# Kernel optimization log

Hardware: AMD Instinct MI355X
Metric: run time of the kernel (lower is better)

The kernel has to match this reference:

```python
import jax, jax.numpy as jnp
import numpy as np

N = 8192
F_IN = 256
F_OUT = 64
ALPHA = 0.2  # leaky-relu negative slope
NEG_INF = -9e15


def setup_inputs() -> dict:
    key = jax.random.key(0)
    k1, k2, k3, k4 = jax.random.split(key, 4)
    h = jax.random.normal(k1, (N, F_IN), dtype=jnp.float32)
    adj = jax.random.randint(k2, (N, N), 0, 2, dtype=jnp.int32)
    W = jax.random.normal(k3, (F_IN, F_OUT), dtype=jnp.float32)
    a = jax.random.normal(k4, (2 * F_OUT, 1), dtype=jnp.float32)
    return {"h": h, "adj": adj, "W": W, "a": a}


def reference(h, adj, W, a):
    # Wh: [N, F_OUT]
    Wh = h @ W
    # Decompose a = [a1; a2]: e_ij = leakyrelu(a1^T Wh_i + a2^T Wh_j),
    # identical math to concat([Wh_i, Wh_j]) @ a without the O(N^2*2F) tensor.
    a1 = a[:F_OUT, 0]
    a2 = a[F_OUT:, 0]
    s1 = Wh @ a1  # [N]
    s2 = Wh @ a2  # [N]
    e = s1[:, None] + s2[None, :]  # [N, N]
    e = jnp.where(e > 0, e, ALPHA * e)  # leaky relu
    scores = jnp.where(adj > 0, e, NEG_INF)
    attention = jax.nn.softmax(scores, axis=1)  # [N, N]
    h_prime = attention @ Wh  # [N, F_OUT]
    return h_prime
```

## Files before the change

kernel.cpp:

```cpp
#include <hip/hip_runtime.h>

#define N 8192
#define F_IN 256
#define F_OUT 64
#define ALPHA 0.2f
#define LOG2E 1.4426950408889634f
#define NEGBIG -3.0e38f
#define MINIT -1.0e30f

typedef __attribute__((ext_vector_type(8))) short bf16x8;
typedef __attribute__((ext_vector_type(4))) float f32x4;
typedef __attribute__((ext_vector_type(4))) int i32x4;
typedef __attribute__((ext_vector_type(4))) unsigned u32x4;
typedef __attribute__((ext_vector_type(4))) unsigned short u16x4;

__device__ __forceinline__ unsigned short f2bf(float x) {
    unsigned u = __float_as_uint(x);
    u = (u + 0x7FFFu + ((u >> 16) & 1u)) >> 16;
    return (unsigned short)u;
}
__device__ __forceinline__ float bf2f(unsigned short h) {
    return __uint_as_float((unsigned)h << 16);
}
__device__ __forceinline__ float fast_exp2(float x) {
#if __has_builtin(__builtin_amdgcn_exp2f)
    return __builtin_amdgcn_exp2f(x);
#else
    return __expf(x * 0.6931471805599453f);
#endif
}
__device__ __forceinline__ i32x4 ntload4(const int* p) {
    return __builtin_nontemporal_load((const i32x4*)p);
}

__global__ __launch_bounds__(256) void prep_kernel(
    const float* __restrict__ W, const float* __restrict__ a,
    float* __restrict__ Wa1, float* __restrict__ Wa2,
    unsigned short* __restrict__ WbTh, unsigned short* __restrict__ WbTl) {
    __shared__ float Wl[F_IN][F_OUT + 1];
    __shared__ float al[2 * F_OUT];
    const int t = threadIdx.x;
    for (int it = 0; it < 16; ++it) {
        const int idx = it * 1024 + t * 4;
        const f32x4 v = *(const f32x4*)&W[idx];
        const int r = idx >> 6, c = idx & 63;
        Wl[r][c] = v[0]; Wl[r][c + 1] = v[1]; Wl[r][c + 2] = v[2]; Wl[r][c + 3] = v[3];
    }
    if (t < 128) al[t] = a[t];
    __syncthreads();
    float x1 = 0.f, x2 = 0.f;
#pragma unroll 8
    for (int f = 0; f < F_OUT; ++f) {
        const float wv = Wl[t][f];
        x1 += wv * al[f];
        x2 += wv * al[F_OUT + f];
    }
    Wa1[t] = x1; Wa2[t] = x2;
    const int f = t >> 2, k0 = (t & 3) * 64;
    for (int kk = 0; kk < 64; kk += 8) {
        u32x4 ph, pl;
#pragma unroll
        for (int u = 0; u < 4; ++u) {
            const float w0 = Wl[k0 + kk + 2 * u][f];
            const float w1 = Wl[k0 + kk + 2 * u + 1][f];
            const unsigned short h0 = f2bf(w0), h1 = f2bf(w1);
            const unsigned short l0 = f2bf(w0 - bf2f(h0)), l1 = f2bf(w1 - bf2f(h1));
            ph[u] = (unsigned)h0 | ((unsigned)h1 << 16);
            pl[u] = (unsigned)l0 | ((unsigned)l1 << 16);
        }
        *(u32x4*)&WbTh[f * F_IN + k0 + kk] = ph;
        *(u32x4*)&WbTl[f * F_IN + k0 + kk] = pl;
    }
}

__global__ __launch_bounds__(256) void score_kernel(
    const float* __restrict__ h, const float* __restrict__ Wa1,
    const float* __restrict__ Wa2, float* __restrict__ s1c, float* __restrict__ s2c) {
    __shared__ float w1l[F_IN], w2l[F_IN];
    const int t = threadIdx.x, wave = t >> 6, lane = t & 63;
    w1l[t] = Wa1[t]; w2l[t] = Wa2[t];
    __syncthreads();
    const int row0 = blockIdx.x * 16 + wave * 4;
    const f32x4 wa1 = *(const f32x4*)&w1l[lane * 4];
    const f32x4 wa2 = *(const f32x4*)&w2l[lane * 4];
#pragma unroll
    for (int r = 0; r < 4; ++r) {
        const f32x4 hv = *(const f32x4*)(h + (size_t)(row0 + r) * F_IN + lane * 4);
        float d1 = hv[0] * wa1[0] + hv[1] * wa1[1] + hv[2] * wa1[2] + hv[3] * wa1[3];
        float d2 = hv[0] * wa2[0] + hv[1] * wa2[1] + hv[2] * wa2[2] + hv[3] * wa2[3];
#pragma unroll
        for (int off = 32; off; off >>= 1) {
            d1 += __shfl_down(d1, off, 64);
            d2 += __shfl_down(d2, off, 64);
        }
        if (lane == 0) { s1c[row0 + r] = d1 * LOG2E; s2c[row0 + r] = d2 * LOG2E; }
    }
}

__global__ __launch_bounds__(256) void whT_kernel(
    const float* __restrict__ h, const unsigned short* __restrict__ WbTh,
    const unsigned short* __restrict__ WbTl, unsigned short* __restrict__ WhT) {
    const int t = threadIdx.x;
    const int nt = t >> 6, lane = t & 63;
    const int mq = lane & 15, quad = lane >> 4;
    const int i0 = blockIdx.x * 16;
    const float* hp = h + (size_t)(i0 + mq) * F_IN + quad * 8;
    const unsigned short* bph = WbTh + (nt * 16 + mq) * F_IN + quad * 8;
    const unsigned short* bpl = WbTl + (nt * 16 + mq) * F_IN + quad * 8;
    f32x4 acc = {0.f, 0.f, 0.f, 0.f};
#pragma unroll
    for (int kk = 0; kk < 8; ++kk) {
        const f32x4 h0 = *(const f32x4*)(hp + kk * 32);
        const f32x4 h1 = *(const f32x4*)(hp + kk * 32 + 4);
        bf16x8 ah, al;
#pragma unroll
        for (int u = 0; u < 8; ++u) {
            const float v = (u < 4) ? h0[u] : h1[u - 4];
            const unsigned short hi = f2bf(v);
            ah[u] = (short)hi;
            al[u] = (short)f2bf(v - bf2f(hi));
        }
        const bf16x8 bh = *(const bf16x8*)(bph + kk * 32);
        const bf16x8 bl = *(const bf16x8*)(bpl + kk * 32);
        acc = __builtin_amdgcn_mfma_f32_16x16x32_bf16(ah, bh, acc, 0, 0, 0);
        acc = __builtin_amdgcn_mfma_f32_16x16x32_bf16(al, bh, acc, 0, 0, 0);
        acc = __builtin_amdgcn_mfma_f32_16x16x32_bf16(ah, bl, acc, 0, 0, 0);
    }
    u16x4 o;
#pragma unroll
    for (int r = 0; r < 4; ++r) o[r] = f2bf(acc[r]);
    *(u16x4*)&WhT[(size_t)(nt * 16 + mq) * N + i0 + quad * 4] = o;
}

#define AROWS 16
__global__ __launch_bounds__(512, 4) void attn_kernel(
    const int* __restrict__ adj,
    const unsigned short* __restrict__ WhT,
    const float* __restrict__ s1c, const float* __restrict__ s2c,
    float* __restrict__ out) {
    __shared__ float s1l[AROWS];
    __shared__ __align__(16) float accbuf[8][AROWS][F_OUT];
    __shared__ float rowsums[8][AROWS];
    __shared__ float rowmaxs[8][AROWS];

    const int t = threadIdx.x, wave = t >> 6, lane = t & 63;
    const int i0 = blockIdx.x * AROWS;
    if (t < AROWS) s1l[t] = s1c[i0 + t];
    __syncthreads();

    const int mq = lane & 15, quad = lane >> 4;
    const float s1m = s1l[mq];
    const int jb0 = wave * 1024;

    const int* __restrict__ ap = adj + (size_t)(i0 + mq) * N + jb0 + quad * 8;
    const float* __restrict__ sp = s2c + jb0 + quad * 8;
    const unsigned short* __restrict__ wp = WhT + (size_t)mq * N + jb0 + quad * 8;

    f32x4 acc0 = {0.f, 0.f, 0.f, 0.f}, acc1 = acc0, acc2 = acc0, acc3 = acc0, accS = acc0;
    bf16x8 onesf;
#pragma unroll
    for (int u = 0; u < 8; ++u) onesf[u] = (mq == 0) ? (short)0x3F80 : (short)0;

    float m = MINIT;
    i32x4 a0 = ntload4(ap);
    i32x4 a1 = ntload4(ap + 4);

#pragma unroll 2
    for (int c = 0; c < 32; ++c) {
        i32x4 na0 = a0, na1 = a1;
        if (c + 1 < 32) {
            na0 = ntload4(ap + (c + 1) * 32);
            na1 = ntload4(ap + (c + 1) * 32 + 4);
        }
        const f32x4 v0 = *(const f32x4*)(sp + c * 32);
        const f32x4 v1 = *(const f32x4*)(sp + c * 32 + 4);
        const unsigned short* wpc = wp + c * 32;
        const bf16x8 b0 = *(const bf16x8*)(wpc);
        const bf16x8 b1 = *(const bf16x8*)(wpc + 16 * N);
        const bf16x8 b2 = *(const bf16x8*)(wpc + 32 * N);
        const bf16x8 b3 = *(const bf16x8*)(wpc + 48 * N);

        float es[8];
        float tm = NEGBIG;
#pragma unroll
        for (int jj = 0; jj < 8; ++jj) {
            const float s2k = (jj < 4) ? v0[jj] : v1[jj - 4];
            const float x = s1m + s2k;
            const float e = fmaxf(x, ALPHA * x);
            const int av = (jj < 4) ? a0[jj] : a1[jj - 4];
            const float sel = (av > 0) ? e : NEGBIG;
            es[jj] = sel;
            tm = fmaxf(tm, sel);
        }
        tm = fmaxf(tm, __shfl_xor(tm, 16, 64));
        tm = fmaxf(tm, __shfl_xor(tm, 32, 64));
        const float nm = fmaxf(m, tm);
        const float f = fast_exp2(m - nm);
        m = nm;
        float fr0 = __shfl(f, quad * 4 + 0, 64);
        float fr1 = __shfl(f, quad * 4 + 1, 64);
        float fr2 = __shfl(f, quad * 4 + 2, 64);
        float fr3 = __shfl(f, quad * 4 + 3, 64);
        acc0[0] *= fr0; acc1[0] *= fr0; acc2[0] *= fr0; acc3[0] *= fr0; accS[0] *= fr0;
        acc0[1] *= fr1; acc1[1] *= fr1; acc2[1] *= fr1; acc3[1] *= fr1; accS[1] *= fr1;
        acc0[2] *= fr2; acc1[2] *= fr2; acc2[2] *= fr2; acc3[2] *= fr2; accS[2] *= fr2;
        acc0[3] *= fr3; acc1[3] *= fr3; acc2[3] *= fr3; acc3[3] *= fr3; accS[3] *= fr3;

        bf16x8 af;
#pragma unroll
        for (int jj = 0; jj < 8; ++jj) {
            const float w = fast_exp2(es[jj] - m);
            af[jj] = (short)(__float_as_uint(w) >> 16);
        }
        acc0 = __builtin_amdgcn_mfma_f32_16x16x32_bf16(af, b0, acc0, 0, 0, 0);
        acc1 = __builtin_amdgcn_mfma_f32_16x16x32_bf16(af, b1, acc1, 0, 0, 0);
        acc2 = __builtin_amdgcn_mfma_f32_16x16x32_bf16(af, b2, acc2, 0, 0, 0);
        acc3 = __builtin_amdgcn_mfma_f32_16x16x32_bf16(af, b3, acc3, 0, 0, 0);
        accS = __builtin_amdgcn_mfma_f32_16x16x32_bf16(af, onesf, accS, 0, 0, 0);
        a0 = na0; a1 = na1;
    }

#pragma unroll
    for (int r = 0; r < 4; ++r) {
        const int row = quad * 4 + r;
        accbuf[wave][row][0 + mq]  = acc0[r];
        accbuf[wave][row][16 + mq] = acc1[r];
        accbuf[wave][row][32 + mq] = acc2[r];
        accbuf[wave][row][48 + mq] = acc3[r];
        if (mq == 0) rowsums[wave][row] = accS[r];
    }
    if (lane < AROWS) rowmaxs[wave][lane] = m;
    __syncthreads();

    {
        const int row = t >> 5, f0 = (t & 31) * 2;
        float M = rowmaxs[0][row];
#pragma unroll
        for (int w = 1; w < 8; ++w) M = fmaxf(M, rowmaxs[w][row]);
        float o0 = 0.f, o1 = 0.f, rs = 0.f;
#pragma unroll
        for (int w = 0; w < 8; ++w) {
            const float fw = fast_exp2(rowmaxs[w][row] - M);
            o0 += accbuf[w][row][f0] * fw;
            o1 += accbuf[w][row][f0 + 1] * fw;
            rs += rowsums[w][row] * fw;
        }
        const float inv = (rs > 0.f) ? 1.f / rs : 0.f;
        float2 st = {o0 * inv, o1 * inv};
        *(float2*)&out[(size_t)(i0 + row) * F_OUT + f0] = st;
    }
}

extern "C" void kernel_launch(void* const* d_in, const int* in_sizes, int n_in,
                              void* d_out, int out_size, void* d_ws, size_t ws_size,
                              hipStream_t stream) {
    const float* h   = (const float*)d_in[0];
    const int*   adj = (const int*)d_in[1];
    const float* W   = (const float*)d_in[2];
    const float* a   = (const float*)d_in[3];
    float* out = (float*)d_out;

    char* ws = (char*)d_ws;
    unsigned short* WhT = (unsigned short*)ws;
    float* s1c  = (float*)(ws + (size_t)F_OUT * N * 2);
    float* s2c  = s1c + N;
    float* Wa1  = s2c + N;
    float* Wa2  = Wa1 + F_IN;
    unsigned short* WbTh = (unsigned short*)(Wa2 + F_IN);
    unsigned short* WbTl = WbTh + F_OUT * F_IN;

    prep_kernel<<<1, 256, 0, stream>>>(W, a, Wa1, Wa2, WbTh, WbTl);
    score_kernel<<<N / 16, 256, 0, stream>>>(h, Wa1, Wa2, s1c, s2c);
    whT_kernel<<<N / 16, 256, 0, stream>>>(h, WbTh, WbTl, WhT);
    attn_kernel<<<N / AROWS, 512, 0, stream>>>(adj, WhT, s1c, s2c, out);
}
```

Baseline: 440.8 us.

## Replace online softmax max with precomputed global s2 max bound

The score kernel now computes a global maximum of s2 with an order-preserving-key atomicMax. The attention kernel uses it to derive a fixed per-row upper bound on the leaky-relu score (minus an offset). This removes the running-max tracking, cross-lane shuffles and accumulator rescaling from the inner loop, and the cross-wave max merge at the end. The adjacency prefetch also goes two chunks ahead instead of one. The risk is underflow: masked-in entries far below the bound can flush to zero, which depends on the score range of the inputs.

```diff
diff --git a/kernel.cpp b/kernel.cpp
--- a/kernel.cpp
+++ b/kernel.cpp
@@ -5,8 +5,7 @@
 #define F_OUT 64
 #define ALPHA 0.2f
 #define LOG2E 1.4426950408889634f
-#define NEGBIG -3.0e38f
-#define MINIT -1.0e30f
+#define COFF 80.0f
 
 typedef __attribute__((ext_vector_type(8))) short bf16x8;
 typedef __attribute__((ext_vector_type(4))) float f32x4;
@@ -29,6 +28,14 @@
     return __expf(x * 0.6931471805599453f);
 #endif
 }
+__device__ __forceinline__ unsigned fkey(float x) {
+    unsigned u = __float_as_uint(x);
+    return ((int)u < 0) ? ~u : (u | 0x80000000u);
+}
+__device__ __forceinline__ float funkey(unsigned k) {
+    unsigned u = (k & 0x80000000u) ? (k & 0x7FFFFFFFu) : ~k;
+    return __uint_as_float(u);
+}
 __device__ __forceinline__ i32x4 ntload4(const int* p) {
     return __builtin_nontemporal_load((const i32x4*)p);
 }
@@ -36,10 +43,12 @@
 __global__ __launch_bounds__(256) void prep_kernel(
     const float* __restrict__ W, const float* __restrict__ a,
     float* __restrict__ Wa1, float* __restrict__ Wa2,
-    unsigned short* __restrict__ WbTh, unsigned short* __restrict__ WbTl) {
+    unsigned short* __restrict__ WbTh, unsigned short* __restrict__ WbTl,
+    unsigned* __restrict__ maxkey) {
     __shared__ float Wl[F_IN][F_OUT + 1];
     __shared__ float al[2 * F_OUT];
     const int t = threadIdx.x;
+    if (t == 0) *maxkey = 0u;
     for (int it = 0; it < 16; ++it) {
         const int idx = it * 1024 + t * 4;
         const f32x4 v = *(const f32x4*)&W[idx];
@@ -75,14 +84,17 @@
 
 __global__ __launch_bounds__(256) void score_kernel(
     const float* __restrict__ h, const float* __restrict__ Wa1,
-    const float* __restrict__ Wa2, float* __restrict__ s1c, float* __restrict__ s2c) {
+    const float* __restrict__ Wa2, float* __restrict__ s1c, float* __restrict__ s2c,
+    unsigned* __restrict__ maxkey) {
     __shared__ float w1l[F_IN], w2l[F_IN];
+    __shared__ float red[4];
     const int t = threadIdx.x, wave = t >> 6, lane = t & 63;
     w1l[t] = Wa1[t]; w2l[t] = Wa2[t];
     __syncthreads();
     const int row0 = blockIdx.x * 16 + wave * 4;
     const f32x4 wa1 = *(const f32x4*)&w1l[lane * 4];
     const f32x4 wa2 = *(const f32x4*)&w2l[lane * 4];
+    float wmax = -3.0e38f;
 #pragma unroll
     for (int r = 0; r < 4; ++r) {
         const f32x4 hv = *(const f32x4*)(h + (size_t)(row0 + r) * F_IN + lane * 4);
@@ -93,7 +105,17 @@
             d1 += __shfl_down(d1, off, 64);
             d2 += __shfl_down(d2, off, 64);
         }
-        if (lane == 0) { s1c[row0 + r] = d1 * LOG2E; s2c[row0 + r] = d2 * LOG2E; }
+        if (lane == 0) {
+            const float v2 = d2 * LOG2E;
+            s1c[row0 + r] = d1 * LOG2E; s2c[row0 + r] = v2;
+            wmax = fmaxf(wmax, v2);
+        }
+    }
+    if (lane == 0) red[wave] = wmax;
+    __syncthreads();
+    if (t == 0) {
+        const float bm = fmaxf(fmaxf(red[0], red[1]), fmaxf(red[2], red[3]));
+        atomicMax(maxkey, fkey(bm));
     }
 }
 
@@ -137,11 +159,10 @@
     const int* __restrict__ adj,
     const unsigned short* __restrict__ WhT,
     const float* __restrict__ s1c, const float* __restrict__ s2c,
-    float* __restrict__ out) {
+    const unsigned* __restrict__ maxkey, float* __restrict__ out) {
     __shared__ float s1l[AROWS];
     __shared__ __align__(16) float accbuf[8][AROWS][F_OUT];
     __shared__ float rowsums[8][AROWS];
-    __shared__ float rowmaxs[8][AROWS];
 
     const int t = threadIdx.x, wave = t >> 6, lane = t & 63;
     const int i0 = blockIdx.x * AROWS;
@@ -150,6 +171,11 @@
 
     const int mq = lane & 15, quad = lane >> 4;
     const float s1m = s1l[mq];
+    const float maxS2 = funkey(*maxkey);
+    const float xb = s1m + maxS2;
+    const float Bc = fmaxf(xb, ALPHA * xb) - COFF;
+    const float c1 = s1m - Bc;
+    const float c2 = ALPHA * s1m - Bc;
     const int jb0 = wave * 1024;
 
     const int* __restrict__ ap = adj + (size_t)(i0 + mq) * N + jb0 + quad * 8;
@@ -161,16 +187,15 @@
 #pragma unroll
     for (int u = 0; u < 8; ++u) onesf[u] = (mq == 0) ? (short)0x3F80 : (short)0;
 
-    float m = MINIT;
-    i32x4 a0 = ntload4(ap);
-    i32x4 a1 = ntload4(ap + 4);
+    i32x4 a0c = ntload4(ap),      a1c = ntload4(ap + 4);
+    i32x4 a0n = ntload4(ap + 32), a1n = ntload4(ap + 36);
 
 #pragma unroll 2
     for (int c = 0; c < 32; ++c) {
-        i32x4 na0 = a0, na1 = a1;
-        if (c + 1 < 32) {
-            na0 = ntload4(ap + (c + 1) * 32);
-            na1 = ntload4(ap + (c + 1) * 32 + 4);
+        i32x4 a0f = a0n, a1f = a1n;
+        if (c + 2 < 32) {
+            a0f = ntload4(ap + (c + 2) * 32);
+            a1f = ntload4(ap + (c + 2) * 32 + 4);
         }
         const f32x4 v0 = *(const f32x4*)(sp + c * 32);
         const f32x4 v1 = *(const f32x4*)(sp + c * 32 + 4);
@@ -180,36 +205,15 @@
         const bf16x8 b2 = *(const bf16x8*)(wpc + 32 * N);
         const bf16x8 b3 = *(const bf16x8*)(wpc + 48 * N);
 
-        float es[8];
-        float tm = NEGBIG;
+        bf16x8 af;
 #pragma unroll
         for (int jj = 0; jj < 8; ++jj) {
             const float s2k = (jj < 4) ? v0[jj] : v1[jj - 4];
-            const float x = s1m + s2k;
-            const float e = fmaxf(x, ALPHA * x);
-            const int av = (jj < 4) ? a0[jj] : a1[jj - 4];
-            const float sel = (av > 0) ? e : NEGBIG;
-            es[jj] = sel;
-            tm = fmaxf(tm, sel);
-        }
-        tm = fmaxf(tm, __shfl_xor(tm, 16, 64));
-        tm = fmaxf(tm, __shfl_xor(tm, 32, 64));
-        const float nm = fmaxf(m, tm);
-        const float f = fast_exp2(m - nm);
-        m = nm;
-        float fr0 = __shfl(f, quad * 4 + 0, 64);
-        float fr1 = __shfl(f, quad * 4 + 1, 64);
-        float fr2 = __shfl(f, quad * 4 + 2, 64);
-        float fr3 = __shfl(f, quad * 4 + 3, 64);
-        acc0[0] *= fr0; acc1[0] *= fr0; acc2[0] *= fr0; acc3[0] *= fr0; accS[0] *= fr0;
-        acc0[1] *= fr1; acc1[1] *= fr1; acc2[1] *= fr1; acc3[1] *= fr1; accS[1] *= fr1;
-        acc0[2] *= fr2; acc1[2] *= fr2; acc2[2] *= fr2; acc3[2] *= fr2; accS[2] *= fr2;
-        acc0[3] *= fr3; acc1[3] *= fr3; acc2[3] *= fr3; acc3[3] *= fr3; accS[3] *= fr3;
-
-        bf16x8 af;
-#pragma unroll
-        for (int jj = 0; jj < 8; ++jj) {
-            const float w = fast_exp2(es[jj] - m);
+            const float p = c1 + s2k;
+            const float q = __builtin_fmaf(ALPHA, s2k, c2);
+            const float e = fmaxf(p, q);
+            const int av = (jj < 4) ? a0c[jj] : a1c[jj - 4];
+            const float w = (av > 0) ? fast_exp2(e) : 0.f;
             af[jj] = (short)(__float_as_uint(w) >> 16);
         }
         acc0 = __builtin_amdgcn_mfma_f32_16x16x32_bf16(af, b0, acc0, 0, 0, 0);
@@ -217,7 +221,7 @@
         acc2 = __builtin_amdgcn_mfma_f32_16x16x32_bf16(af, b2, acc2, 0, 0, 0);
         acc3 = __builtin_amdgcn_mfma_f32_16x16x32_bf16(af, b3, acc3, 0, 0, 0);
         accS = __builtin_amdgcn_mfma_f32_16x16x32_bf16(af, onesf, accS, 0, 0, 0);
-        a0 = na0; a1 = na1;
+        a0c = a0n; a1c = a1n; a0n = a0f; a1n = a1f;
     }
 
 #pragma unroll
@@ -229,21 +233,16 @@
         accbuf[wave][row][48 + mq] = acc3[r];
         if (mq == 0) rowsums[wave][row] = accS[r];
     }
-    if (lane < AROWS) rowmaxs[wave][lane] = m;
     __syncthreads();
 
     {
         const int row = t >> 5, f0 = (t & 31) * 2;
-        float M = rowmaxs[0][row];
-#pragma unroll
-        for (int w = 1; w < 8; ++w) M = fmaxf(M, rowmaxs[w][row]);
         float o0 = 0.f, o1 = 0.f, rs = 0.f;
 #pragma unroll
         for (int w = 0; w < 8; ++w) {
-            const float fw = fast_exp2(rowmaxs[w][row] - M);
-            o0 += accbuf[w][row][f0] * fw;
-            o1 += accbuf[w][row][f0 + 1] * fw;
-            rs += rowsums[w][row] * fw;
+            o0 += accbuf[w][row][f0];
+            o1 += accbuf[w][row][f0 + 1];
+            rs += rowsums[w][row];
         }
         const float inv = (rs > 0.f) ? 1.f / rs : 0.f;
         float2 st = {o0 * inv, o1 * inv};
@@ -268,9 +267,10 @@
     float* Wa2  = Wa1 + F_IN;
     unsigned short* WbTh = (unsigned short*)(Wa2 + F_IN);
     unsigned short* WbTl = WbTh + F_OUT * F_IN;
-
-    prep_kernel<<<1, 256, 0, stream>>>(W, a, Wa1, Wa2, WbTh, WbTl);
-    score_kernel<<<N / 16, 256, 0, stream>>>(h, Wa1, Wa2, s1c, s2c);
+    unsigned* maxkey = (unsigned*)(WbTl + F_OUT * F_IN);
+
+    prep_kernel<<<1, 256, 0, stream>>>(W, a, Wa1, Wa2, WbTh, WbTl, maxkey);
+    score_kernel<<<N / 16, 256, 0, stream>>>(h, Wa1, Wa2, s1c, s2c, maxkey);
     whT_kernel<<<N / 16, 256, 0, stream>>>(h, WbTh, WbTl, WhT);
-    attn_kernel<<<N / AROWS, 512, 0, stream>>>(adj, WhT, s1c, s2c, out);
-}
+    attn_kernel<<<N / AROWS, 512, 0, stream>>>(adj, WhT, s1c, s2c, maxkey, out);
+}
```

New measurement: 445.5 us. No clear change (+1.1%).
